# Performance work log

Hardware: AMD Instinct MI355X
Metric: run time of the kernel (lower is better)

## Reference

```python
import jax, jax.numpy as jnp
import numpy as np

MEMORY_SIZE = 8192
FEATURE_DIM = 512
NUM_QUERIES = 32768
EPS = 1e-12  # guard for sqrt in cdist


def setup_inputs() -> dict:
    key = jax.random.key(0)
    k1, k2, k3, k4 = jax.random.split(key, 4)
    return {
        "features": jax.random.normal(k1, (MEMORY_SIZE, FEATURE_DIM), dtype=jnp.float32),
        "positions": jax.random.normal(k2, (MEMORY_SIZE, 3), dtype=jnp.float32),
        "query_positions": jax.random.normal(k3, (NUM_QUERIES, 3), dtype=jnp.float32),
        "position_embeddings": jax.random.normal(k4, (MEMORY_SIZE, 3), dtype=jnp.float32),
    }


def _cdist(a, b):
    # Euclidean distance via ||a||^2 + ||b||^2 - 2 a.b; avoids [Q,M,3] intermediate.
    a2 = jnp.sum(a * a, axis=-1, keepdims=True)          # [Q,1]
    b2 = jnp.sum(b * b, axis=-1, keepdims=True).T        # [1,M]
    d2 = a2 + b2 - 2.0 * (a @ b.T)                       # [Q,M]
    return jnp.sqrt(jnp.maximum(d2, EPS))


def reference(features, positions, query_positions, position_embeddings):
    # --- update ---
    positions_norm = positions / jnp.linalg.norm(positions, axis=-1, keepdims=True)
    embeddings_norm = position_embeddings / jnp.linalg.norm(position_embeddings, axis=-1, keepdims=True)
    sim = positions_norm @ embeddings_norm.T             # [M,M]
    attn = jax.nn.softmax(sim, axis=-1)
    memory = attn @ features                              # [M,F]
    new_pos_emb = attn @ positions                        # [M,3]
    # --- query ---
    dist = _cdist(query_positions, new_pos_emb)           # [Q,M]
    qattn = jax.nn.softmax(-dist, axis=-1)
    retrieved = qattn @ memory                            # [Q,F]
    return retrieved
```

## Files before the change

### kernel.cpp

```cpp
#include <hip/hip_runtime.h>
#include <stdint.h>
#include <stddef.h>

#define M_SZ 8192
#define F_DIM 512
#define N_Q 32768

typedef __attribute__((ext_vector_type(4))) float f32x4;
typedef __attribute__((ext_vector_type(8))) __bf16 bf16x8;
typedef __attribute__((ext_vector_type(2))) __bf16 bf16x2;

__device__ __forceinline__ float bits_to_f(unsigned u) {
    union { unsigned u; float f; } v; v.u = u; return v.f;
}
__device__ __forceinline__ unsigned pk_bf16(float a, float b) {
    union { bf16x2 v; unsigned u; } cv;
    cv.v.x = (__bf16)a; cv.v.y = (__bf16)b;
    return cv.u;
}
__device__ __forceinline__ unsigned short f2bf(float x) {
    union { bf16x2 v; unsigned u; } cv;
    cv.v.x = (__bf16)x; cv.v.y = (__bf16)0.0f;
    return (unsigned short)(cv.u & 0xffffu);
}
__device__ __forceinline__ bf16x8 as_bf16x8(uint4 u) {
    union { uint4 a; bf16x8 b; } cv; cv.a = u; return cv.b;
}

__global__ void prep_kernel(const float* __restrict__ pos,
                            const float* __restrict__ emb,
                            float* __restrict__ pn4,
                            float* __restrict__ en4,
                            float* __restrict__ pos4) {
    int i = blockIdx.x * 256 + threadIdx.x;
    if (i >= M_SZ) return;
    float x = pos[i * 3 + 0], y = pos[i * 3 + 1], z = pos[i * 3 + 2];
    float inv = 1.0f / __builtin_amdgcn_sqrtf(x * x + y * y + z * z);
    pn4[i * 4 + 0] = x * inv; pn4[i * 4 + 1] = y * inv;
    pn4[i * 4 + 2] = z * inv; pn4[i * 4 + 3] = 0.0f;
    pos4[i * 4 + 0] = x; pos4[i * 4 + 1] = y;
    pos4[i * 4 + 2] = z; pos4[i * 4 + 3] = 0.0f;
    float ex = emb[i * 3 + 0], ey = emb[i * 3 + 1], ez = emb[i * 3 + 2];
    float einv = 1.0f / __builtin_amdgcn_sqrtf(ex * ex + ey * ey + ez * ez);
    en4[i * 4 + 0] = ex * einv; en4[i * 4 + 1] = ey * einv;
    en4[i * 4 + 2] = ez * einv; en4[i * 4 + 3] = 0.0f;
}

__global__ void transpose_kernel(const float* __restrict__ feat,
                                 unsigned short* __restrict__ featT) {
    __shared__ float tile[64 * 65];
    const int jb = blockIdx.x * 64, fb = blockIdx.y * 64;
    const int t = threadIdx.x;
#pragma unroll
    for (int p = 0; p < 16; ++p) {
        int idx = p * 256 + t;
        int j = idx >> 6, f = idx & 63;
        tile[j * 65 + f] = feat[(size_t)(jb + j) * F_DIM + fb + f];
    }
    __syncthreads();
#pragma unroll
    for (int p = 0; p < 16; ++p) {
        int idx = p * 256 + t;
        int f = idx >> 6, j = idx & 63;
        featT[(size_t)(fb + f) * M_SZ + jb + j] = f2bf(tile[j * 65 + f]);
    }
}

__launch_bounds__(512, 2)
__global__ void build_memory_kernel(const float* __restrict__ pn4,
                                    const float* __restrict__ en4,
                                    const float* __restrict__ pos4,
                                    const unsigned short* __restrict__ featT,
                                    unsigned short* __restrict__ memT,
                                    float* __restrict__ npe4) {
    constexpr int BM = 32, BK = 32, PSTR = BK + 8;
    __shared__ unsigned short pbuf[2][BM * PSTR];
    __shared__ f32x4 red4[512];
    __shared__ float lbuf[BM];

    const int t = threadIdx.x;
    const int lane = t & 63, wv = t >> 6;
    const int col = lane & 15, quad = lane >> 4;
    const int mb = blockIdx.x * BM;
    const int r = t & 31, jq = t >> 5;

    const f32x4 pnr = ((const f32x4*)pn4)[mb + r];
    const f32x4* en = (const f32x4*)en4;
    const f32x4* ps = (const f32x4*)pos4;

    const unsigned short* bp[4];
#pragma unroll
    for (int n = 0; n < 4; ++n)
        bp[n] = featT + (size_t)(wv * 64 + n * 16 + col) * M_SZ + quad * 8;

    f32x4 acc[2][4];
    const f32x4 zero4 = {0.f, 0.f, 0.f, 0.f};
#pragma unroll
    for (int m = 0; m < 2; ++m)
#pragma unroll
        for (int n = 0; n < 4; ++n) acc[m][n] = zero4;
    float nx = 0.f, ny = 0.f, nz = 0.f, lp = 0.f;

    uint4 vbA[4], vbB[4];
#pragma unroll
    for (int n = 0; n < 4; ++n) vbA[n] = *(const uint4*)(bp[n]);

#define B_GEN_P(JB, SIDE)                                                    \
    {                                                                        \
        int j = (JB) + jq * 2;                                               \
        f32x4 e0 = en[j], e1 = en[j + 1];                                    \
        f32x4 p0 = ps[j], p1 = ps[j + 1];                                    \
        float s0 = fmaf(pnr.x, e0.x, fmaf(pnr.y, e0.y, pnr.z * e0.z));       \
        float s1 = fmaf(pnr.x, e1.x, fmaf(pnr.y, e1.y, pnr.z * e1.z));       \
        float w0 = __builtin_amdgcn_exp2f(s0 * 1.44269504f);                 \
        float w1 = __builtin_amdgcn_exp2f(s1 * 1.44269504f);                 \
        unsigned u = pk_bf16(w0, w1);                                        \
        float w0r = bits_to_f(u << 16), w1r = bits_to_f(u & 0xffff0000u);    \
        lp += w0r + w1r;                                                     \
        nx = fmaf(w0r, p0.x, fmaf(w1r, p1.x, nx));                           \
        ny = fmaf(w0r, p0.y, fmaf(w1r, p1.y, ny));                           \
        nz = fmaf(w0r, p0.z, fmaf(w1r, p1.z, nz));                           \
        *(unsigned*)(&pbuf[SIDE][r * PSTR + jq * 2]) = u;                    \
    }

#define B_MFMA(VB, SIDE)                                                     \
    {                                                                        \
        _Pragma("unroll") for (int m = 0; m < 2; ++m) {                      \
            bf16x8 a = *(const bf16x8*)(&pbuf[SIDE][(m * 16 + col) * PSTR + quad * 8]); \
            _Pragma("unroll") for (int n = 0; n < 4; ++n)                    \
                acc[m][n] = __builtin_amdgcn_mfma_f32_16x16x32_bf16(         \
                    a, as_bf16x8(VB[n]), acc[m][n], 0, 0, 0);                \
        }                                                                    \
    }

#define B_BODY(CUR, NXT, SIDE, JNXT)                                         \
    {                                                                        \
        _Pragma("unroll") for (int n = 0; n < 4; ++n) {                      \
            NXT[n] = *(const uint4*)(bp[n] + BK);                            \
            bp[n] += BK;                                                     \
        }                                                                    \
        B_GEN_P(JNXT, SIDE ^ 1)                                              \
        B_MFMA(CUR, SIDE)                                                    \
        __syncthreads();                                                     \
    }

    B_GEN_P(0, 0)
    __syncthreads();

    int jn = BK;
    for (int kt = 0; kt < 254; kt += 2) {
        B_BODY(vbA, vbB, 0, jn) jn += BK;
        B_BODY(vbB, vbA, 1, jn) jn += BK;
    }
    B_BODY(vbA, vbB, 0, jn)
    B_MFMA(vbB, 1)
#undef B_BODY
#undef B_MFMA
#undef B_GEN_P

    f32x4 mine = {nx, ny, nz, lp};
    red4[t] = mine;
    __syncthreads();
    if (t < BM) {
        f32x4 s = red4[t];
#pragma unroll
        for (int g = 1; g < 16; ++g) {
            f32x4 o = red4[t + 32 * g];
            s.x += o.x; s.y += o.y; s.z += o.z; s.w += o.w;
        }
        lbuf[t] = s.w;
        float inv = 1.0f / s.w;
        float X = s.x * inv, Y = s.y * inv, Z = s.z * inv;
        f32x4 o = {X, Y, Z, X * X + Y * Y + Z * Z};
        ((f32x4*)npe4)[mb + t] = o;
    }
    __syncthreads();

#pragma unroll
    for (int m = 0; m < 2; ++m) {
        f32x4 l4 = *(const f32x4*)(lbuf + m * 16 + quad * 4);
        f32x4 inv4 = {1.0f / l4.x, 1.0f / l4.y, 1.0f / l4.z, 1.0f / l4.w};
        int mg = mb + m * 16 + quad * 4;
#pragma unroll
        for (int n = 0; n < 4; ++n) {
            int fg = wv * 64 + n * 16 + col;
            uint2 o;
            o.x = pk_bf16(acc[m][n].x * inv4.x, acc[m][n].y * inv4.y);
            o.y = pk_bf16(acc[m][n].z * inv4.z, acc[m][n].w * inv4.w);
            *(uint2*)(memT + (size_t)fg * M_SZ + mg) = o;
        }
    }
}

__launch_bounds__(512, 2)
__global__ void query_kernel(const float* __restrict__ qpos,
                             const float* __restrict__ npe4,
                             const unsigned short* __restrict__ memT,
                             float* __restrict__ out) {
    constexpr int BM = 128, BK = 32, PSTR = BK + 8;
    __shared__ unsigned short pbuf[2][BM * PSTR];
    __shared__ float redl[512];
    __shared__ float lbuf[BM];

    const int t = threadIdx.x;
    const int lane = t & 63, wv = t >> 6;
    const int col = lane & 15, quad = lane >> 4;
    const int qb = blockIdx.x * BM;
    const int r = t & 127, jq = t >> 7;

    const float qx = qpos[(size_t)(qb + r) * 3 + 0];
    const float qy = qpos[(size_t)(qb + r) * 3 + 1];
    const float qz = qpos[(size_t)(qb + r) * 3 + 2];
    const float q2 = qx * qx + qy * qy + qz * qz;
    const float m2x = -2.0f * qx, m2y = -2.0f * qy, m2z = -2.0f * qz;

    const f32x4* nsrc = (const f32x4*)npe4;

    const unsigned short* bp[4];
#pragma unroll
    for (int n = 0; n < 4; ++n)
        bp[n] = memT + (size_t)(wv * 64 + n * 16 + col) * M_SZ + quad * 8;

    f32x4 acc[8][4];
    const f32x4 zero4 = {0.f, 0.f, 0.f, 0.f};
#pragma unroll
    for (int m = 0; m < 8; ++m)
#pragma unroll
        for (int n = 0; n < 4; ++n) acc[m][n] = zero4;
    float lp = 0.f;

    uint4 vbA[4], vbB[4];
#pragma unroll
    for (int n = 0; n < 4; ++n) vbA[n] = *(const uint4*)(bp[n]);

#define Q_GEN_P(JB, SIDE)                                                    \
    {                                                                        \
        unsigned pk4[4];                                                     \
        _Pragma("unroll") for (int i = 0; i < 8; i += 2) {                   \
            int j = (JB) + jq * 8 + i;                                       \
            f32x4 n0 = nsrc[j], n1 = nsrc[j + 1];                            \
            float s0 = fmaf(m2x, n0.x, fmaf(m2y, n0.y, fmaf(m2z, n0.z, q2 + n0.w))); \
            float s1 = fmaf(m2x, n1.x, fmaf(m2y, n1.y, fmaf(m2z, n1.z, q2 + n1.w))); \
            s0 = fmaxf(s0, 1e-12f); s1 = fmaxf(s1, 1e-12f);                  \
            float w0 = __builtin_amdgcn_exp2f(__builtin_amdgcn_sqrtf(s0) * -1.44269504f); \
            float w1 = __builtin_amdgcn_exp2f(__builtin_amdgcn_sqrtf(s1) * -1.44269504f); \
            unsigned u = pk_bf16(w0, w1);                                    \
            lp += bits_to_f(u << 16) + bits_to_f(u & 0xffff0000u);           \
            pk4[i >> 1] = u;                                                 \
        }                                                                    \
        *(uint4*)(&pbuf[SIDE][r * PSTR + jq * 8]) =                          \
            make_uint4(pk4[0], pk4[1], pk4[2], pk4[3]);                      \
    }

#define Q_MFMA(VB, SIDE)                                                     \
    {                                                                        \
        _Pragma("unroll") for (int m = 0; m < 8; ++m) {                      \
            bf16x8 a = *(const bf16x8*)(&pbuf[SIDE][(m * 16 + col) * PSTR + quad * 8]); \
            _Pragma("unroll") for (int n = 0; n < 4; ++n)                    \
                acc[m][n] = __builtin_amdgcn_mfma_f32_16x16x32_bf16(         \
                    a, as_bf16x8(VB[n]), acc[m][n], 0, 0, 0);                \
        }                                                                    \
    }

#define Q_BODY(CUR, NXT, SIDE, JNXT)                                         \
    {                                                                        \
        _Pragma("unroll") for (int n = 0; n < 4; ++n) {                      \
            NXT[n] = *(const uint4*)(bp[n] + BK);                            \
            bp[n] += BK;                                                     \
        }                                                                    \
        Q_GEN_P(JNXT, SIDE ^ 1)                                              \
        Q_MFMA(CUR, SIDE)                                                    \
        __syncthreads();                                                     \
    }

    Q_GEN_P(0, 0)
    __syncthreads();

    int jn = BK;
    for (int kt = 0; kt < 254; kt += 2) {
        Q_BODY(vbA, vbB, 0, jn) jn += BK;
        Q_BODY(vbB, vbA, 1, jn) jn += BK;
    }
    Q_BODY(vbA, vbB, 0, jn)
    Q_MFMA(vbB, 1)
#undef Q_BODY
#undef Q_MFMA
#undef Q_GEN_P

    redl[t] = lp;
    __syncthreads();
    if (t < BM) lbuf[t] = redl[t] + redl[t + 128] + redl[t + 256] + redl[t + 384];
    __syncthreads();

#pragma unroll
    for (int m = 0; m < 8; ++m) {
        f32x4 l4 = *(const f32x4*)(lbuf + m * 16 + quad * 4);
        f32x4 inv4 = {1.0f / l4.x, 1.0f / l4.y, 1.0f / l4.z, 1.0f / l4.w};
        int qg = qb + m * 16 + quad * 4;
#pragma unroll
        for (int n = 0; n < 4; ++n) {
            int fg = wv * 64 + n * 16 + col;
            out[(size_t)(qg + 0) * F_DIM + fg] = acc[m][n].x * inv4.x;
            out[(size_t)(qg + 1) * F_DIM + fg] = acc[m][n].y * inv4.y;
            out[(size_t)(qg + 2) * F_DIM + fg] = acc[m][n].z * inv4.z;
            out[(size_t)(qg + 3) * F_DIM + fg] = acc[m][n].w * inv4.w;
        }
    }
}

extern "C" void kernel_launch(void* const* d_in, const int* in_sizes, int n_in,
                              void* d_out, int out_size, void* d_ws, size_t ws_size,
                              hipStream_t stream) {
    const float* features  = (const float*)d_in[0];
    const float* positions = (const float*)d_in[1];
    const float* qpos      = (const float*)d_in[2];
    const float* pemb      = (const float*)d_in[3];
    float* out = (float*)d_out;
    char* ws = (char*)d_ws;

    unsigned short* featT = (unsigned short*)(ws);
    unsigned short* memT  = (unsigned short*)(ws + 8388608);
    float* npe4 = (float*)(ws + 16777216);
    float* pn4  = (float*)(ws + 16908288);
    float* en4  = (float*)(ws + 17039360);
    float* pos4 = (float*)(ws + 17170432);

    hipLaunchKernelGGL(prep_kernel, dim3(M_SZ / 256), dim3(256), 0, stream,
                       positions, pemb, pn4, en4, pos4);
    hipLaunchKernelGGL(transpose_kernel, dim3(M_SZ / 64, F_DIM / 64), dim3(256), 0, stream,
                       features, featT);
    hipLaunchKernelGGL(build_memory_kernel, dim3(M_SZ / 32), dim3(512), 0, stream,
                       pn4, en4, pos4, featT, memT, npe4);
    hipLaunchKernelGGL(query_kernel, dim3(N_Q / 128), dim3(512), 0, stream,
                       qpos, npe4, memT, out);
}
```

Measured before the change: 816.3 us.

## Generate softmax A-fragments in registers and split feature dim across blocks

Both the memory-build and query kernels no longer stage the exponentiated attention weights through double-buffered LDS. Each wave now computes its own MFMA A-fragment directly in registers, which removes the per-k-step barriers and LDS round trips. The output tile is re-partitioned: each block covers half the feature dimension and more rows, and the grid doubles. The cost is that the exp/sqrt weight generation is recomputed redundantly per feature-half and per wave. The query kernel also holds 32 accumulators per thread, which raises register pressure and may cut occupancy.

```diff
diff --git a/kernel.cpp b/kernel.cpp
--- a/kernel.cpp
+++ b/kernel.cpp
@@ -25,6 +25,9 @@
 }
 __device__ __forceinline__ bf16x8 as_bf16x8(uint4 u) {
     union { uint4 a; bf16x8 b; } cv; cv.a = u; return cv.b;
+}
+__device__ __forceinline__ bf16x8 mk_bf16x8(unsigned a, unsigned b, unsigned c, unsigned d) {
+    union { uint4 a; bf16x8 b; } cv; cv.a = make_uint4(a, b, c, d); return cv.b;
 }
 
 __global__ void prep_kernel(const float* __restrict__ pos,
@@ -73,120 +76,118 @@
                                     const unsigned short* __restrict__ featT,
                                     unsigned short* __restrict__ memT,
                                     float* __restrict__ npe4) {
-    constexpr int BM = 32, BK = 32, PSTR = BK + 8;
-    __shared__ unsigned short pbuf[2][BM * PSTR];
-    __shared__ f32x4 red4[512];
-    __shared__ float lbuf[BM];
+    __shared__ float lbuf[64];
 
     const int t = threadIdx.x;
-    const int lane = t & 63, wv = t >> 6;
-    const int col = lane & 15, quad = lane >> 4;
-    const int mb = blockIdx.x * BM;
-    const int r = t & 31, jq = t >> 5;
-
-    const f32x4 pnr = ((const f32x4*)pn4)[mb + r];
+    const int wvid = t >> 6, l = t & 63;
+    const int wm = wvid >> 2, wn = wvid & 3;
+    const int col = l & 15, quad = l >> 4;
+    const int bid = blockIdx.x;
+    const int fb = bid & 1;
+    const int mb = (bid >> 1) * 64;
+
     const f32x4* en = (const f32x4*)en4;
     const f32x4* ps = (const f32x4*)pos4;
 
-    const unsigned short* bp[4];
-#pragma unroll
-    for (int n = 0; n < 4; ++n)
-        bp[n] = featT + (size_t)(wv * 64 + n * 16 + col) * M_SZ + quad * 8;
+    f32x4 pnc[2];
+#pragma unroll
+    for (int mf = 0; mf < 2; ++mf)
+        pnc[mf] = ((const f32x4*)pn4)[mb + (wm * 2 + mf) * 16 + col];
+
+    const bool donpe = (fb == 0) && (wn == 0);
+
+    const unsigned short* bB =
+        featT + (size_t)(fb * 256 + wn * 64 + col) * M_SZ + quad * 8;
 
     f32x4 acc[2][4];
     const f32x4 zero4 = {0.f, 0.f, 0.f, 0.f};
 #pragma unroll
-    for (int m = 0; m < 2; ++m)
-#pragma unroll
-        for (int n = 0; n < 4; ++n) acc[m][n] = zero4;
-    float nx = 0.f, ny = 0.f, nz = 0.f, lp = 0.f;
-
-    uint4 vbA[4], vbB[4];
-#pragma unroll
-    for (int n = 0; n < 4; ++n) vbA[n] = *(const uint4*)(bp[n]);
-
-#define B_GEN_P(JB, SIDE)                                                    \
-    {                                                                        \
-        int j = (JB) + jq * 2;                                               \
-        f32x4 e0 = en[j], e1 = en[j + 1];                                    \
-        f32x4 p0 = ps[j], p1 = ps[j + 1];                                    \
-        float s0 = fmaf(pnr.x, e0.x, fmaf(pnr.y, e0.y, pnr.z * e0.z));       \
-        float s1 = fmaf(pnr.x, e1.x, fmaf(pnr.y, e1.y, pnr.z * e1.z));       \
-        float w0 = __builtin_amdgcn_exp2f(s0 * 1.44269504f);                 \
-        float w1 = __builtin_amdgcn_exp2f(s1 * 1.44269504f);                 \
-        unsigned u = pk_bf16(w0, w1);                                        \
-        float w0r = bits_to_f(u << 16), w1r = bits_to_f(u & 0xffff0000u);    \
-        lp += w0r + w1r;                                                     \
-        nx = fmaf(w0r, p0.x, fmaf(w1r, p1.x, nx));                           \
-        ny = fmaf(w0r, p0.y, fmaf(w1r, p1.y, ny));                           \
-        nz = fmaf(w0r, p0.z, fmaf(w1r, p1.z, nz));                           \
-        *(unsigned*)(&pbuf[SIDE][r * PSTR + jq * 2]) = u;                    \
-    }
-
-#define B_MFMA(VB, SIDE)                                                     \
-    {                                                                        \
-        _Pragma("unroll") for (int m = 0; m < 2; ++m) {                      \
-            bf16x8 a = *(const bf16x8*)(&pbuf[SIDE][(m * 16 + col) * PSTR + quad * 8]); \
-            _Pragma("unroll") for (int n = 0; n < 4; ++n)                    \
-                acc[m][n] = __builtin_amdgcn_mfma_f32_16x16x32_bf16(         \
-                    a, as_bf16x8(VB[n]), acc[m][n], 0, 0, 0);                \
-        }                                                                    \
-    }
-
-#define B_BODY(CUR, NXT, SIDE, JNXT)                                         \
-    {                                                                        \
-        _Pragma("unroll") for (int n = 0; n < 4; ++n) {                      \
-            NXT[n] = *(const uint4*)(bp[n] + BK);                            \
-            bp[n] += BK;                                                     \
-        }                                                                    \
-        B_GEN_P(JNXT, SIDE ^ 1)                                              \
-        B_MFMA(CUR, SIDE)                                                    \
-        __syncthreads();                                                     \
-    }
-
-    B_GEN_P(0, 0)
+    for (int mf = 0; mf < 2; ++mf)
+#pragma unroll
+        for (int nf = 0; nf < 4; ++nf) acc[mf][nf] = zero4;
+    float lp2[2] = {0.f, 0.f};
+    float nxa[2] = {0.f, 0.f}, nya[2] = {0.f, 0.f}, nza[2] = {0.f, 0.f};
+
+    for (int kt = 0; kt < 256; ++kt) {
+        const int k0 = kt * 32 + quad * 8;
+        uint4 vb[4];
+#pragma unroll
+        for (int nf = 0; nf < 4; ++nf)
+            vb[nf] = *(const uint4*)(bB + (size_t)nf * 16 * M_SZ + kt * 32);
+        f32x4 ee[8];
+#pragma unroll
+        for (int i = 0; i < 8; ++i) ee[i] = en[k0 + i];
+
+        bf16x8 af[2];
+#pragma unroll
+        for (int mf = 0; mf < 2; ++mf) {
+            unsigned au[4];
+#pragma unroll
+            for (int i = 0; i < 8; i += 2) {
+                float s0 = fmaf(pnc[mf].x, ee[i].x,
+                           fmaf(pnc[mf].y, ee[i].y, pnc[mf].z * ee[i].z));
+                float s1 = fmaf(pnc[mf].x, ee[i + 1].x,
+                           fmaf(pnc[mf].y, ee[i + 1].y, pnc[mf].z * ee[i + 1].z));
+                float w0 = __builtin_amdgcn_exp2f(s0 * 1.44269504f);
+                float w1 = __builtin_amdgcn_exp2f(s1 * 1.44269504f);
+                unsigned u = pk_bf16(w0, w1);
+                au[i >> 1] = u;
+                float w0r = bits_to_f(u << 16), w1r = bits_to_f(u & 0xffff0000u);
+                lp2[mf] += w0r + w1r;
+                if (donpe) {
+                    f32x4 p0 = ps[k0 + i], p1 = ps[k0 + i + 1];
+                    nxa[mf] = fmaf(w0r, p0.x, fmaf(w1r, p1.x, nxa[mf]));
+                    nya[mf] = fmaf(w0r, p0.y, fmaf(w1r, p1.y, nya[mf]));
+                    nza[mf] = fmaf(w0r, p0.z, fmaf(w1r, p1.z, nza[mf]));
+                }
+            }
+            af[mf] = mk_bf16x8(au[0], au[1], au[2], au[3]);
+        }
+#pragma unroll
+        for (int nf = 0; nf < 4; ++nf) {
+            acc[0][nf] = __builtin_amdgcn_mfma_f32_16x16x32_bf16(
+                af[0], as_bf16x8(vb[nf]), acc[0][nf], 0, 0, 0);
+            acc[1][nf] = __builtin_amdgcn_mfma_f32_16x16x32_bf16(
+                af[1], as_bf16x8(vb[nf]), acc[1][nf], 0, 0, 0);
+        }
+    }
+
+    float lsum[2];
+#pragma unroll
+    for (int mf = 0; mf < 2; ++mf) {
+        float s = lp2[mf];
+        s += __shfl_xor(s, 16);
+        s += __shfl_xor(s, 32);
+        lsum[mf] = s;
+        if (quad == 0 && wn == 0) lbuf[(wm * 2 + mf) * 16 + col] = s;
+    }
+    if (donpe) {
+#pragma unroll
+        for (int mf = 0; mf < 2; ++mf) {
+            float sx = nxa[mf]; sx += __shfl_xor(sx, 16); sx += __shfl_xor(sx, 32);
+            float sy = nya[mf]; sy += __shfl_xor(sy, 16); sy += __shfl_xor(sy, 32);
+            float sz = nza[mf]; sz += __shfl_xor(sz, 16); sz += __shfl_xor(sz, 32);
+            if (quad == 0) {
+                float inv = 1.0f / lsum[mf];
+                float X = sx * inv, Y = sy * inv, Z = sz * inv;
+                f32x4 o = {X, Y, Z, X * X + Y * Y + Z * Z};
+                ((f32x4*)npe4)[mb + (wm * 2 + mf) * 16 + col] = o;
+            }
+        }
+    }
     __syncthreads();
 
-    int jn = BK;
-    for (int kt = 0; kt < 254; kt += 2) {
-        B_BODY(vbA, vbB, 0, jn) jn += BK;
-        B_BODY(vbB, vbA, 1, jn) jn += BK;
-    }
-    B_BODY(vbA, vbB, 0, jn)
-    B_MFMA(vbB, 1)
-#undef B_BODY
-#undef B_MFMA
-#undef B_GEN_P
-
-    f32x4 mine = {nx, ny, nz, lp};
-    red4[t] = mine;
-    __syncthreads();
-    if (t < BM) {
-        f32x4 s = red4[t];
-#pragma unroll
-        for (int g = 1; g < 16; ++g) {
-            f32x4 o = red4[t + 32 * g];
-            s.x += o.x; s.y += o.y; s.z += o.z; s.w += o.w;
-        }
-        lbuf[t] = s.w;
-        float inv = 1.0f / s.w;
-        float X = s.x * inv, Y = s.y * inv, Z = s.z * inv;
-        f32x4 o = {X, Y, Z, X * X + Y * Y + Z * Z};
-        ((f32x4*)npe4)[mb + t] = o;
-    }
-    __syncthreads();
-
-#pragma unroll
-    for (int m = 0; m < 2; ++m) {
-        f32x4 l4 = *(const f32x4*)(lbuf + m * 16 + quad * 4);
+#pragma unroll
+    for (int mf = 0; mf < 2; ++mf) {
+        f32x4 l4 = *(const f32x4*)(lbuf + (wm * 2 + mf) * 16 + quad * 4);
         f32x4 inv4 = {1.0f / l4.x, 1.0f / l4.y, 1.0f / l4.z, 1.0f / l4.w};
-        int mg = mb + m * 16 + quad * 4;
-#pragma unroll
-        for (int n = 0; n < 4; ++n) {
-            int fg = wv * 64 + n * 16 + col;
+        int mg = mb + (wm * 2 + mf) * 16 + quad * 4;
+#pragma unroll
+        for (int nf = 0; nf < 4; ++nf) {
+            int fg = fb * 256 + (wn * 4 + nf) * 16 + col;
             uint2 o;
-            o.x = pk_bf16(acc[m][n].x * inv4.x, acc[m][n].y * inv4.y);
-            o.y = pk_bf16(acc[m][n].z * inv4.z, acc[m][n].w * inv4.w);
+            o.x = pk_bf16(acc[mf][nf].x * inv4.x, acc[mf][nf].y * inv4.y);
+            o.y = pk_bf16(acc[mf][nf].z * inv4.z, acc[mf][nf].w * inv4.w);
             *(uint2*)(memT + (size_t)fg * M_SZ + mg) = o;
         }
     }
@@ -197,113 +198,109 @@
                              const float* __restrict__ npe4,
                              const unsigned short* __restrict__ memT,
                              float* __restrict__ out) {
-    constexpr int BM = 128, BK = 32, PSTR = BK + 8;
-    __shared__ unsigned short pbuf[2][BM * PSTR];
-    __shared__ float redl[512];
-    __shared__ float lbuf[BM];
+    __shared__ float lbuf[256];
 
     const int t = threadIdx.x;
-    const int lane = t & 63, wv = t >> 6;
-    const int col = lane & 15, quad = lane >> 4;
-    const int qb = blockIdx.x * BM;
-    const int r = t & 127, jq = t >> 7;
-
-    const float qx = qpos[(size_t)(qb + r) * 3 + 0];
-    const float qy = qpos[(size_t)(qb + r) * 3 + 1];
-    const float qz = qpos[(size_t)(qb + r) * 3 + 2];
-    const float q2 = qx * qx + qy * qy + qz * qz;
-    const float m2x = -2.0f * qx, m2y = -2.0f * qy, m2z = -2.0f * qz;
+    const int wv = t >> 6, l = t & 63;
+    const int col = l & 15, quad = l >> 4;
+    const int bid = blockIdx.x;
+    const int fb = bid & 1;
+    const int qb = (bid >> 1) * 256;
+
+    float m2x[2], m2y[2], m2z[2], q2c[2];
+#pragma unroll
+    for (int mf = 0; mf < 2; ++mf) {
+        int r = qb + (wv * 2 + mf) * 16 + col;
+        float qx = qpos[(size_t)r * 3 + 0];
+        float qy = qpos[(size_t)r * 3 + 1];
+        float qz = qpos[(size_t)r * 3 + 2];
+        q2c[mf] = qx * qx + qy * qy + qz * qz;
+        m2x[mf] = -2.0f * qx; m2y[mf] = -2.0f * qy; m2z[mf] = -2.0f * qz;
+    }
 
     const f32x4* nsrc = (const f32x4*)npe4;
-
-    const unsigned short* bp[4];
-#pragma unroll
-    for (int n = 0; n < 4; ++n)
-        bp[n] = memT + (size_t)(wv * 64 + n * 16 + col) * M_SZ + quad * 8;
-
-    f32x4 acc[8][4];
+    const unsigned short* bB =
+        memT + (size_t)(fb * 256 + col) * M_SZ + quad * 8;
+
+    f32x4 acc[2][16];
     const f32x4 zero4 = {0.f, 0.f, 0.f, 0.f};
 #pragma unroll
-    for (int m = 0; m < 8; ++m)
-#pragma unroll
-        for (int n = 0; n < 4; ++n) acc[m][n] = zero4;
-    float lp = 0.f;
-
-    uint4 vbA[4], vbB[4];
-#pragma unroll
-    for (int n = 0; n < 4; ++n) vbA[n] = *(const uint4*)(bp[n]);
-
-#define Q_GEN_P(JB, SIDE)                                                    \
-    {                                                                        \
-        unsigned pk4[4];                                                     \
-        _Pragma("unroll") for (int i = 0; i < 8; i += 2) {                   \
-            int j = (JB) + jq * 8 + i;                                       \
-            f32x4 n0 = nsrc[j], n1 = nsrc[j + 1];                            \
-            float s0 = fmaf(m2x, n0.x, fmaf(m2y, n0.y, fmaf(m2z, n0.z, q2 + n0.w))); \
-            float s1 = fmaf(m2x, n1.x, fmaf(m2y, n1.y, fmaf(m2z, n1.z, q2 + n1.w))); \
-            s0 = fmaxf(s0, 1e-12f); s1 = fmaxf(s1, 1e-12f);                  \
-            float w0 = __builtin_amdgcn_exp2f(__builtin_amdgcn_sqrtf(s0) * -1.44269504f); \
-            float w1 = __builtin_amdgcn_exp2f(__builtin_amdgcn_sqrtf(s1) * -1.44269504f); \
-            unsigned u = pk_bf16(w0, w1);                                    \
-            lp += bits_to_f(u << 16) + bits_to_f(u & 0xffff0000u);           \
-            pk4[i >> 1] = u;                                                 \
-        }                                                                    \
-        *(uint4*)(&pbuf[SIDE][r * PSTR + jq * 8]) =                          \
-            make_uint4(pk4[0], pk4[1], pk4[2], pk4[3]);                      \
-    }
-
-#define Q_MFMA(VB, SIDE)                                                     \
-    {                                                                        \
-        _Pragma("unroll") for (int m = 0; m < 8; ++m) {                      \
-            bf16x8 a = *(const bf16x8*)(&pbuf[SIDE][(m * 16 + col) * PSTR + quad * 8]); \
-            _Pragma("unroll") for (int n = 0; n < 4; ++n)                    \
-                acc[m][n] = __builtin_amdgcn_mfma_f32_16x16x32_bf16(         \
-                    a, as_bf16x8(VB[n]), acc[m][n], 0, 0, 0);                \
-        }                                                                    \
-    }
-
-#define Q_BODY(CUR, NXT, SIDE, JNXT)                                         \
-    {                                                                        \
-        _Pragma("unroll") for (int n = 0; n < 4; ++n) {                      \
-            NXT[n] = *(const uint4*)(bp[n] + BK);                            \
-            bp[n] += BK;                                                     \
-        }                                                                    \
-        Q_GEN_P(JNXT, SIDE ^ 1)                                              \
-        Q_MFMA(CUR, SIDE)                                                    \
-        __syncthreads();                                                     \
-    }
-
-    Q_GEN_P(0, 0)
+    for (int mf = 0; mf < 2; ++mf)
+#pragma unroll
+        for (int nf = 0; nf < 16; ++nf) acc[mf][nf] = zero4;
+    float lp2[2] = {0.f, 0.f};
+
+    for (int kt = 0; kt < 256; ++kt) {
+        const int k0 = kt * 32 + quad * 8;
+        uint4 vb[8];
+#pragma unroll
+        for (int nf = 0; nf < 8; ++nf)
+            vb[nf] = *(const uint4*)(bB + (size_t)nf * 16 * M_SZ + kt * 32);
+        f32x4 nn[8];
+#pragma unroll
+        for (int i = 0; i < 8; ++i) nn[i] = nsrc[k0 + i];
+
+        bf16x8 af[2];
+#pragma unroll
+        for (int mf = 0; mf < 2; ++mf) {
+            unsigned au[4];
+#pragma unroll
+            for (int i = 0; i < 8; i += 2) {
+                float s0 = fmaf(m2x[mf], nn[i].x, fmaf(m2y[mf], nn[i].y,
+                           fmaf(m2z[mf], nn[i].z, q2c[mf] + nn[i].w)));
+                float s1 = fmaf(m2x[mf], nn[i + 1].x, fmaf(m2y[mf], nn[i + 1].y,
+                           fmaf(m2z[mf], nn[i + 1].z, q2c[mf] + nn[i + 1].w)));
+                s0 = fmaxf(s0, 1e-12f); s1 = fmaxf(s1, 1e-12f);
+                float w0 = __builtin_amdgcn_exp2f(
+                    __builtin_amdgcn_sqrtf(s0) * -1.44269504f);
+                float w1 = __builtin_amdgcn_exp2f(
+                    __builtin_amdgcn_sqrtf(s1) * -1.44269504f);
+                unsigned u = pk_bf16(w0, w1);
+                au[i >> 1] = u;
+                lp2[mf] += bits_to_f(u << 16) + bits_to_f(u & 0xffff0000u);
+            }
+            af[mf] = mk_bf16x8(au[0], au[1], au[2], au[3]);
+        }
+#pragma unroll
+        for (int nf = 0; nf < 8; ++nf) {
+            acc[0][nf] = __builtin_amdgcn_mfma_f32_16x16x32_bf16(
+                af[0], as_bf16x8(vb[nf]), acc[0][nf], 0, 0, 0);
+            acc[1][nf] = __builtin_amdgcn_mfma_f32_16x16x32_bf16(
+                af[1], as_bf16x8(vb[nf]), acc[1][nf], 0, 0, 0);
+        }
+#pragma unroll
+        for (int nf = 0; nf < 8; ++nf)
+            vb[nf] = *(const uint4*)(bB + (size_t)(8 + nf) * 16 * M_SZ + kt * 32);
+#pragma unroll
+        for (int nf = 0; nf < 8; ++nf) {
+            acc[0][8 + nf] = __builtin_amdgcn_mfma_f32_16x16x32_bf16(
+                af[0], as_bf16x8(vb[nf]), acc[0][8 + nf], 0, 0, 0);
+            acc[1][8 + nf] = __builtin_amdgcn_mfma_f32_16x16x32_bf16(
+                af[1], as_bf16x8(vb[nf]), acc[1][8 + nf], 0, 0, 0);
+        }
+    }
+
+#pragma unroll
+    for (int mf = 0; mf < 2; ++mf) {
+        float s = lp2[mf];
+        s += __shfl_xor(s, 16);
+        s += __shfl_xor(s, 32);
+        if (quad == 0) lbuf[(wv * 2 + mf) * 16 + col] = s;
+    }
     __syncthreads();
 
-    int jn = BK;
-    for (int kt = 0; kt < 254; kt += 2) {
-        Q_BODY(vbA, vbB, 0, jn) jn += BK;
-        Q_BODY(vbB, vbA, 1, jn) jn += BK;
-    }
-    Q_BODY(vbA, vbB, 0, jn)
-    Q_MFMA(vbB, 1)
-#undef Q_BODY
-#undef Q_MFMA
-#undef Q_GEN_P
-
-    redl[t] = lp;
-    __syncthreads();
-    if (t < BM) lbuf[t] = redl[t] + redl[t + 128] + redl[t + 256] + redl[t + 384];
-    __syncthreads();
-
-#pragma unroll
-    for (int m = 0; m < 8; ++m) {
-        f32x4 l4 = *(const f32x4*)(lbuf + m * 16 + quad * 4);
+#pragma unroll
+    for (int mf = 0; mf < 2; ++mf) {
+        f32x4 l4 = *(const f32x4*)(lbuf + (wv * 2 + mf) * 16 + quad * 4);
         f32x4 inv4 = {1.0f / l4.x, 1.0f / l4.y, 1.0f / l4.z, 1.0f / l4.w};
-        int qg = qb + m * 16 + quad * 4;
-#pragma unroll
-        for (int n = 0; n < 4; ++n) {
-            int fg = wv * 64 + n * 16 + col;
-            out[(size_t)(qg + 0) * F_DIM + fg] = acc[m][n].x * inv4.x;
-            out[(size_t)(qg + 1) * F_DIM + fg] = acc[m][n].y * inv4.y;
-            out[(size_t)(qg + 2) * F_DIM + fg] = acc[m][n].z * inv4.z;
-            out[(size_t)(qg + 3) * F_DIM + fg] = acc[m][n].w * inv4.w;
+        int qg = qb + (wv * 2 + mf) * 16 + quad * 4;
+#pragma unroll
+        for (int nf = 0; nf < 16; ++nf) {
+            int fg = fb * 256 + nf * 16 + col;
+            out[(size_t)(qg + 0) * F_DIM + fg] = acc[mf][nf].x * inv4.x;
+            out[(size_t)(qg + 1) * F_DIM + fg] = acc[mf][nf].y * inv4.y;
+            out[(size_t)(qg + 2) * F_DIM + fg] = acc[mf][nf].z * inv4.z;
+            out[(size_t)(qg + 3) * F_DIM + fg] = acc[mf][nf].w * inv4.w;
         }
     }
 }
@@ -329,8 +326,8 @@
                        positions, pemb, pn4, en4, pos4);
     hipLaunchKernelGGL(transpose_kernel, dim3(M_SZ / 64, F_DIM / 64), dim3(256), 0, stream,
                        features, featT);
-    hipLaunchKernelGGL(build_memory_kernel, dim3(M_SZ / 32), dim3(512), 0, stream,
+    hipLaunchKernelGGL(build_memory_kernel, dim3((M_SZ / 64) * 2), dim3(512), 0, stream,
                        pn4, en4, pos4, featT, memT, npe4);
-    hipLaunchKernelGGL(query_kernel, dim3(N_Q / 128), dim3(512), 0, stream,
+    hipLaunchKernelGGL(query_kernel, dim3((N_Q / 256) * 2), dim3(512), 0, stream,
                        qpos, npe4, memT, out);
 }
```

After: 1.848 ms. +126.4%, slower.

## Split feature dimension across blocks and use swizzled LDS layout for P tiles

Applied to the files above, without the earlier changes.

Both GEMM kernels now use 256-thread blocks and split the feature dimension across blocks: four feature slices per 64-row tile in build_memory and two per 128-query tile in query_kernel. This gives more blocks and less per-block work. The P tile in LDS is stored in a fragment-ordered layout without padding, so the MFMA A-operand loads become contiguous per lane. The cost is that the exp/softmax weight computation is repeated in every feature slice: 4x in build and 2x in query. Only the first slice writes the new position embeddings.

```diff
diff --git a/kernel.cpp b/kernel.cpp
--- a/kernel.cpp
+++ b/kernel.cpp
@@ -66,78 +66,88 @@
     }
 }
 
-__launch_bounds__(512, 2)
+__launch_bounds__(256, 2)
 __global__ void build_memory_kernel(const float* __restrict__ pn4,
                                     const float* __restrict__ en4,
                                     const float* __restrict__ pos4,
                                     const unsigned short* __restrict__ featT,
                                     unsigned short* __restrict__ memT,
                                     float* __restrict__ npe4) {
-    constexpr int BM = 32, BK = 32, PSTR = BK + 8;
-    __shared__ unsigned short pbuf[2][BM * PSTR];
-    __shared__ f32x4 red4[512];
-    __shared__ float lbuf[BM];
+    constexpr int BK = 32;
+    __shared__ unsigned short pbuf[2][64 * 32];
+    __shared__ f32x4 red4[256];
+    __shared__ float lbuf[64];
 
     const int t = threadIdx.x;
-    const int lane = t & 63, wv = t >> 6;
-    const int col = lane & 15, quad = lane >> 4;
-    const int mb = blockIdx.x * BM;
-    const int r = t & 31, jq = t >> 5;
+    const int wv = t >> 6, l = t & 63;
+    const int col = l & 15, quad = l >> 4;
+    const int bid = blockIdx.x;
+    const int fb = bid & 3;
+    const int mb = (bid >> 2) * 64;
+    const int r = t & 63, jq = t >> 6;
 
     const f32x4 pnr = ((const f32x4*)pn4)[mb + r];
     const f32x4* en = (const f32x4*)en4;
     const f32x4* ps = (const f32x4*)pos4;
-
-    const unsigned short* bp[4];
-#pragma unroll
-    for (int n = 0; n < 4; ++n)
-        bp[n] = featT + (size_t)(wv * 64 + n * 16 + col) * M_SZ + quad * 8;
-
-    f32x4 acc[2][4];
+    const bool donpe = (fb == 0);
+
+    const unsigned short* bp[2];
+#pragma unroll
+    for (int nf = 0; nf < 2; ++nf)
+        bp[nf] = featT + (size_t)(fb * 128 + wv * 32 + nf * 16 + col) * M_SZ + quad * 8;
+
+    f32x4 acc[4][2];
     const f32x4 zero4 = {0.f, 0.f, 0.f, 0.f};
 #pragma unroll
-    for (int m = 0; m < 2; ++m)
-#pragma unroll
-        for (int n = 0; n < 4; ++n) acc[m][n] = zero4;
-    float nx = 0.f, ny = 0.f, nz = 0.f, lp = 0.f;
-
-    uint4 vbA[4], vbB[4];
-#pragma unroll
-    for (int n = 0; n < 4; ++n) vbA[n] = *(const uint4*)(bp[n]);
+    for (int mf = 0; mf < 4; ++mf)
+#pragma unroll
+        for (int nf = 0; nf < 2; ++nf) acc[mf][nf] = zero4;
+    float lp = 0.f, nx = 0.f, ny = 0.f, nz = 0.f;
+
+    uint4 vbA[2], vbB[2];
+#pragma unroll
+    for (int nf = 0; nf < 2; ++nf) vbA[nf] = *(const uint4*)(bp[nf]);
 
 #define B_GEN_P(JB, SIDE)                                                    \
     {                                                                        \
-        int j = (JB) + jq * 2;                                               \
-        f32x4 e0 = en[j], e1 = en[j + 1];                                    \
-        f32x4 p0 = ps[j], p1 = ps[j + 1];                                    \
-        float s0 = fmaf(pnr.x, e0.x, fmaf(pnr.y, e0.y, pnr.z * e0.z));       \
-        float s1 = fmaf(pnr.x, e1.x, fmaf(pnr.y, e1.y, pnr.z * e1.z));       \
-        float w0 = __builtin_amdgcn_exp2f(s0 * 1.44269504f);                 \
-        float w1 = __builtin_amdgcn_exp2f(s1 * 1.44269504f);                 \
-        unsigned u = pk_bf16(w0, w1);                                        \
-        float w0r = bits_to_f(u << 16), w1r = bits_to_f(u & 0xffff0000u);    \
-        lp += w0r + w1r;                                                     \
-        nx = fmaf(w0r, p0.x, fmaf(w1r, p1.x, nx));                           \
-        ny = fmaf(w0r, p0.y, fmaf(w1r, p1.y, ny));                           \
-        nz = fmaf(w0r, p0.z, fmaf(w1r, p1.z, nz));                           \
-        *(unsigned*)(&pbuf[SIDE][r * PSTR + jq * 2]) = u;                    \
+        unsigned us[4];                                                      \
+        _Pragma("unroll") for (int i = 0; i < 8; i += 2) {                   \
+            int j = (JB) + jq * 8 + i;                                       \
+            f32x4 e0 = en[j], e1 = en[j + 1];                                \
+            float s0 = fmaf(pnr.x, e0.x, fmaf(pnr.y, e0.y, pnr.z * e0.z));   \
+            float s1 = fmaf(pnr.x, e1.x, fmaf(pnr.y, e1.y, pnr.z * e1.z));   \
+            float w0 = __builtin_amdgcn_exp2f(s0 * 1.44269504f);             \
+            float w1 = __builtin_amdgcn_exp2f(s1 * 1.44269504f);             \
+            unsigned u = pk_bf16(w0, w1);                                    \
+            us[i >> 1] = u;                                                  \
+            float w0r = bits_to_f(u << 16), w1r = bits_to_f(u & 0xffff0000u);\
+            lp += w0r + w1r;                                                 \
+            if (donpe) {                                                     \
+                f32x4 p0 = ps[j], p1 = ps[j + 1];                            \
+                nx = fmaf(w0r, p0.x, fmaf(w1r, p1.x, nx));                   \
+                ny = fmaf(w0r, p0.y, fmaf(w1r, p1.y, ny));                   \
+                nz = fmaf(w0r, p0.z, fmaf(w1r, p1.z, nz));                   \
+            }                                                                \
+        }                                                                    \
+        int c0 = (r >> 4) * 64 + jq * 16 + (r & 15);                         \
+        *(uint4*)(&pbuf[SIDE][c0 * 8]) = make_uint4(us[0], us[1], us[2], us[3]); \
     }
 
 #define B_MFMA(VB, SIDE)                                                     \
     {                                                                        \
-        _Pragma("unroll") for (int m = 0; m < 2; ++m) {                      \
-            bf16x8 a = *(const bf16x8*)(&pbuf[SIDE][(m * 16 + col) * PSTR + quad * 8]); \
-            _Pragma("unroll") for (int n = 0; n < 4; ++n)                    \
-                acc[m][n] = __builtin_amdgcn_mfma_f32_16x16x32_bf16(         \
-                    a, as_bf16x8(VB[n]), acc[m][n], 0, 0, 0);                \
+        _Pragma("unroll") for (int mf = 0; mf < 4; ++mf) {                   \
+            bf16x8 a = *(const bf16x8*)(&pbuf[SIDE][(mf * 64 + l) * 8]);     \
+            _Pragma("unroll") for (int nf = 0; nf < 2; ++nf)                 \
+                acc[mf][nf] = __builtin_amdgcn_mfma_f32_16x16x32_bf16(       \
+                    a, as_bf16x8(VB[nf]), acc[mf][nf], 0, 0, 0);             \
         }                                                                    \
     }
 
 #define B_BODY(CUR, NXT, SIDE, JNXT)                                         \
     {                                                                        \
-        _Pragma("unroll") for (int n = 0; n < 4; ++n) {                      \
-            NXT[n] = *(const uint4*)(bp[n] + BK);                            \
-            bp[n] += BK;                                                     \
+        _Pragma("unroll") for (int nf = 0; nf < 2; ++nf) {                   \
+            NXT[nf] = *(const uint4*)(bp[nf] + BK);                          \
+            bp[nf] += BK;                                                    \
         }                                                                    \
         B_GEN_P(JNXT, SIDE ^ 1)                                              \
         B_MFMA(CUR, SIDE)                                                    \
@@ -161,51 +171,55 @@
     f32x4 mine = {nx, ny, nz, lp};
     red4[t] = mine;
     __syncthreads();
-    if (t < BM) {
+    if (t < 64) {
         f32x4 s = red4[t];
 #pragma unroll
-        for (int g = 1; g < 16; ++g) {
-            f32x4 o = red4[t + 32 * g];
+        for (int g = 1; g < 4; ++g) {
+            f32x4 o = red4[t + 64 * g];
             s.x += o.x; s.y += o.y; s.z += o.z; s.w += o.w;
         }
         lbuf[t] = s.w;
-        float inv = 1.0f / s.w;
-        float X = s.x * inv, Y = s.y * inv, Z = s.z * inv;
-        f32x4 o = {X, Y, Z, X * X + Y * Y + Z * Z};
-        ((f32x4*)npe4)[mb + t] = o;
-    }
-    __syncthreads();
-
-#pragma unroll
-    for (int m = 0; m < 2; ++m) {
-        f32x4 l4 = *(const f32x4*)(lbuf + m * 16 + quad * 4);
+        if (donpe) {
+            float inv = 1.0f / s.w;
+            float X = s.x * inv, Y = s.y * inv, Z = s.z * inv;
+            f32x4 o = {X, Y, Z, X * X + Y * Y + Z * Z};
+            ((f32x4*)npe4)[mb + t] = o;
+        }
+    }
+    __syncthreads();
+
+#pragma unroll
+    for (int mf = 0; mf < 4; ++mf) {
+        f32x4 l4 = *(const f32x4*)(lbuf + mf * 16 + quad * 4);
         f32x4 inv4 = {1.0f / l4.x, 1.0f / l4.y, 1.0f / l4.z, 1.0f / l4.w};
-        int mg = mb + m * 16 + quad * 4;
-#pragma unroll
-        for (int n = 0; n < 4; ++n) {
-            int fg = wv * 64 + n * 16 + col;
+        int mg = mb + mf * 16 + quad * 4;
+#pragma unroll
+        for (int nf = 0; nf < 2; ++nf) {
+            int fg = fb * 128 + wv * 32 + nf * 16 + col;
             uint2 o;
-            o.x = pk_bf16(acc[m][n].x * inv4.x, acc[m][n].y * inv4.y);
-            o.y = pk_bf16(acc[m][n].z * inv4.z, acc[m][n].w * inv4.w);
+            o.x = pk_bf16(acc[mf][nf].x * inv4.x, acc[mf][nf].y * inv4.y);
+            o.y = pk_bf16(acc[mf][nf].z * inv4.z, acc[mf][nf].w * inv4.w);
             *(uint2*)(memT + (size_t)fg * M_SZ + mg) = o;
         }
     }
 }
 
-__launch_bounds__(512, 2)
+__launch_bounds__(256, 2)
 __global__ void query_kernel(const float* __restrict__ qpos,
                              const float* __restrict__ npe4,
                              const unsigned short* __restrict__ memT,
                              float* __restrict__ out) {
-    constexpr int BM = 128, BK = 32, PSTR = BK + 8;
-    __shared__ unsigned short pbuf[2][BM * PSTR];
-    __shared__ float redl[512];
-    __shared__ float lbuf[BM];
+    constexpr int BK = 32;
+    __shared__ unsigned short pbuf[2][128 * 32];
+    __shared__ float redl[256];
+    __shared__ float lbuf[128];
 
     const int t = threadIdx.x;
-    const int lane = t & 63, wv = t >> 6;
-    const int col = lane & 15, quad = lane >> 4;
-    const int qb = blockIdx.x * BM;
+    const int wv = t >> 6, l = t & 63;
+    const int col = l & 15, quad = l >> 4;
+    const int bid = blockIdx.x;
+    const int fb = bid & 1;
+    const int qb = (bid >> 1) * 128;
     const int r = t & 127, jq = t >> 7;
 
     const float qx = qpos[(size_t)(qb + r) * 3 + 0];
@@ -218,26 +232,26 @@
 
     const unsigned short* bp[4];
 #pragma unroll
-    for (int n = 0; n < 4; ++n)
-        bp[n] = memT + (size_t)(wv * 64 + n * 16 + col) * M_SZ + quad * 8;
+    for (int nf = 0; nf < 4; ++nf)
+        bp[nf] = memT + (size_t)(fb * 256 + wv * 64 + nf * 16 + col) * M_SZ + quad * 8;
 
     f32x4 acc[8][4];
     const f32x4 zero4 = {0.f, 0.f, 0.f, 0.f};
 #pragma unroll
-    for (int m = 0; m < 8; ++m)
-#pragma unroll
-        for (int n = 0; n < 4; ++n) acc[m][n] = zero4;
+    for (int mf = 0; mf < 8; ++mf)
+#pragma unroll
+        for (int nf = 0; nf < 4; ++nf) acc[mf][nf] = zero4;
     float lp = 0.f;
 
     uint4 vbA[4], vbB[4];
 #pragma unroll
-    for (int n = 0; n < 4; ++n) vbA[n] = *(const uint4*)(bp[n]);
+    for (int nf = 0; nf < 4; ++nf) vbA[nf] = *(const uint4*)(bp[nf]);
 
 #define Q_GEN_P(JB, SIDE)                                                    \
     {                                                                        \
-        unsigned pk4[4];                                                     \
-        _Pragma("unroll") for (int i = 0; i < 8; i += 2) {                   \
-            int j = (JB) + jq * 8 + i;                                       \
+        unsigned us[8];                                                      \
+        _Pragma("unroll") for (int i = 0; i < 16; i += 2) {                  \
+            int j = (JB) + jq * 16 + i;                                      \
             f32x4 n0 = nsrc[j], n1 = nsrc[j + 1];                            \
             float s0 = fmaf(m2x, n0.x, fmaf(m2y, n0.y, fmaf(m2z, n0.z, q2 + n0.w))); \
             float s1 = fmaf(m2x, n1.x, fmaf(m2y, n1.y, fmaf(m2z, n1.z, q2 + n1.w))); \
@@ -246,27 +260,28 @@
             float w1 = __builtin_amdgcn_exp2f(__builtin_amdgcn_sqrtf(s1) * -1.44269504f); \
             unsigned u = pk_bf16(w0, w1);                                    \
             lp += bits_to_f(u << 16) + bits_to_f(u & 0xffff0000u);           \
-            pk4[i >> 1] = u;                                                 \
-        }                                                                    \
-        *(uint4*)(&pbuf[SIDE][r * PSTR + jq * 8]) =                          \
-            make_uint4(pk4[0], pk4[1], pk4[2], pk4[3]);                      \
+            us[i >> 1] = u;                                                  \
+        }                                                                    \
+        int c0 = (r >> 4) * 64 + jq * 32 + (r & 15);                         \
+        *(uint4*)(&pbuf[SIDE][c0 * 8]) = make_uint4(us[0], us[1], us[2], us[3]); \
+        *(uint4*)(&pbuf[SIDE][(c0 + 16) * 8]) = make_uint4(us[4], us[5], us[6], us[7]); \
     }
 
 #define Q_MFMA(VB, SIDE)                                                     \
     {                                                                        \
-        _Pragma("unroll") for (int m = 0; m < 8; ++m) {                      \
-            bf16x8 a = *(const bf16x8*)(&pbuf[SIDE][(m * 16 + col) * PSTR + quad * 8]); \
-            _Pragma("unroll") for (int n = 0; n < 4; ++n)                    \
-                acc[m][n] = __builtin_amdgcn_mfma_f32_16x16x32_bf16(         \
-                    a, as_bf16x8(VB[n]), acc[m][n], 0, 0, 0);                \
+        _Pragma("unroll") for (int mf = 0; mf < 8; ++mf) {                   \
+            bf16x8 a = *(const bf16x8*)(&pbuf[SIDE][(mf * 64 + l) * 8]);     \
+            _Pragma("unroll") for (int nf = 0; nf < 4; ++nf)                 \
+                acc[mf][nf] = __builtin_amdgcn_mfma_f32_16x16x32_bf16(       \
+                    a, as_bf16x8(VB[nf]), acc[mf][nf], 0, 0, 0);             \
         }                                                                    \
     }
 
 #define Q_BODY(CUR, NXT, SIDE, JNXT)                                         \
     {                                                                        \
-        _Pragma("unroll") for (int n = 0; n < 4; ++n) {                      \
-            NXT[n] = *(const uint4*)(bp[n] + BK);                            \
-            bp[n] += BK;                                                     \
+        _Pragma("unroll") for (int nf = 0; nf < 4; ++nf) {                   \
+            NXT[nf] = *(const uint4*)(bp[nf] + BK);                          \
+            bp[nf] += BK;                                                    \
         }                                                                    \
         Q_GEN_P(JNXT, SIDE ^ 1)                                              \
         Q_MFMA(CUR, SIDE)                                                    \
@@ -289,21 +304,21 @@
 
     redl[t] = lp;
     __syncthreads();
-    if (t < BM) lbuf[t] = redl[t] + redl[t + 128] + redl[t + 256] + redl[t + 384];
-    __syncthreads();
-
-#pragma unroll
-    for (int m = 0; m < 8; ++m) {
-        f32x4 l4 = *(const f32x4*)(lbuf + m * 16 + quad * 4);
+    if (t < 128) lbuf[t] = redl[t] + redl[t + 128];
+    __syncthreads();
+
+#pragma unroll
+    for (int mf = 0; mf < 8; ++mf) {
+        f32x4 l4 = *(const f32x4*)(lbuf + mf * 16 + quad * 4);
         f32x4 inv4 = {1.0f / l4.x, 1.0f / l4.y, 1.0f / l4.z, 1.0f / l4.w};
-        int qg = qb + m * 16 + quad * 4;
-#pragma unroll
-        for (int n = 0; n < 4; ++n) {
-            int fg = wv * 64 + n * 16 + col;
-            out[(size_t)(qg + 0) * F_DIM + fg] = acc[m][n].x * inv4.x;
-            out[(size_t)(qg + 1) * F_DIM + fg] = acc[m][n].y * inv4.y;
-            out[(size_t)(qg + 2) * F_DIM + fg] = acc[m][n].z * inv4.z;
-            out[(size_t)(qg + 3) * F_DIM + fg] = acc[m][n].w * inv4.w;
+        int qg = qb + mf * 16 + quad * 4;
+#pragma unroll
+        for (int nf = 0; nf < 4; ++nf) {
+            int fg = fb * 256 + wv * 64 + nf * 16 + col;
+            out[(size_t)(qg + 0) * F_DIM + fg] = acc[mf][nf].x * inv4.x;
+            out[(size_t)(qg + 1) * F_DIM + fg] = acc[mf][nf].y * inv4.y;
+            out[(size_t)(qg + 2) * F_DIM + fg] = acc[mf][nf].z * inv4.z;
+            out[(size_t)(qg + 3) * F_DIM + fg] = acc[mf][nf].w * inv4.w;
         }
     }
 }
@@ -329,8 +344,8 @@
                        positions, pemb, pn4, en4, pos4);
     hipLaunchKernelGGL(transpose_kernel, dim3(M_SZ / 64, F_DIM / 64), dim3(256), 0, stream,
                        features, featT);
-    hipLaunchKernelGGL(build_memory_kernel, dim3(M_SZ / 32), dim3(512), 0, stream,
+    hipLaunchKernelGGL(build_memory_kernel, dim3((M_SZ / 64) * 4), dim3(256), 0, stream,
                        pn4, en4, pos4, featT, memT, npe4);
-    hipLaunchKernelGGL(query_kernel, dim3(N_Q / 128), dim3(512), 0, stream,
+    hipLaunchKernelGGL(query_kernel, dim3((N_Q / 128) * 2), dim3(256), 0, stream,
                        qpos, npe4, memT, out);
 }
```

Result: slower. 979.6 us (+20.0%).
